# Optimization experiments

Measured on AMD Instinct MI355X. Metric: run time of the kernel, lower is better.

Reference implementation:

```python
import jax, jax.numpy as jnp
import numpy as np

B, T, SD, AD, H, K, HID = 256, 128, 8, 2, 3, 4, 256


def setup_inputs() -> dict:
    key = jax.random.key(0)
    ks = jax.random.split(key, 12)
    inp = {
        "state": jax.random.normal(ks[0], (B, T, SD), dtype=jnp.float32),
        "action": jax.random.normal(ks[1], (B, T, AD), dtype=jnp.float32),
        # Linear(4, 4*H, bias=False): weight (4*H, 4)
        "Wk": jax.random.normal(ks[2], (4 * H, K), dtype=jnp.float32) * 0.1,
        "Wq": jax.random.normal(ks[3], (4 * H, SD + AD), dtype=jnp.float32) * 0.1,
        "Wv": jax.random.normal(ks[4], (4 * H, K), dtype=jnp.float32) * 0.1,
        # MLP: in_dim = 4*H + SD + AD -> HID -> HID -> 1
        "W1": jax.random.normal(ks[5], (HID, 4 * H + SD + AD), dtype=jnp.float32) * 0.05,
        "b1": jnp.zeros((HID,), dtype=jnp.float32),
        "W2": jax.random.normal(ks[6], (HID, HID), dtype=jnp.float32) * 0.05,
        "b2": jnp.zeros((HID,), dtype=jnp.float32),
        "Wout": jax.random.uniform(ks[7], (1, HID), minval=-0.003, maxval=0.003, dtype=jnp.float32),
        "bout": jax.random.uniform(ks[8], (1,), minval=-0.003, maxval=0.003, dtype=jnp.float32),
    }
    return inp


def reference(state, action, Wk, Wq, Wv, W1, b1, W2, b2, Wout, bout):
    q_state = jnp.concatenate([state, action], axis=-1)  # (b, t, sd+ad)
    s = state[:, :, :4]                                   # (b, t, 4)
    b, t, k = s.shape
    h = Wk.shape[0] // k
    # rel_full[b, i, j] = s[b, j] - s[b, i]  (matches torch view/transpose)
    rel_full = s[:, None, :, :] - s[:, :, None, :]        # (b, t, t, 4)
    # drop diagonal (self-pairs): idx[i] = all j != i, in order
    j = jnp.arange(t - 1)
    idx = j[None, :] + (j[None, :] >= jnp.arange(t)[:, None])  # (t, t-1)
    rel = jnp.take_along_axis(rel_full, idx[None, :, :, None], axis=2)  # (b, t, t-1, 4)
    # QKV projections (tiny head dim k=4)
    q = (q_state @ Wq.T).reshape(b, t, h, k)              # (b, t, h, 4)
    keys = (rel @ Wk.T).reshape(b, t, t - 1, h, k)        # (b, t, t-1, h, 4)
    vals = (rel @ Wv.T).reshape(b, t, t - 1, h, k)
    scores = jnp.einsum('bthk,btjhk->bthj', q, keys) / jnp.sqrt(jnp.float32(k))
    w = jax.nn.softmax(scores, axis=-1)                   # over the t-1 neighbors
    x = jnp.einsum('bthj,btjhk->bthk', w, vals).reshape(b, t, h * k)
    x = jnp.concatenate([x, q_state], axis=-1)            # (b, t, h*4 + sd+ad)
    x = jax.nn.relu(x @ W1.T + b1)
    x = jax.nn.relu(x @ W2.T + b2)
    return x @ Wout.T + bout                              # (b, t, 1)
```

## Files before the change

kernel.cpp:

```cpp
#include <hip/hip_runtime.h>
#include <math.h>

#define Bp 256
#define Tp 128
#define SDp 8
#define ADp 2
#define Hp 3
#define Kp 4
#define HIDp 256
#define QDp (SDp + ADp)
#define X1Dp (Hp * Kp + QDp)
#define X1PAD 32
#define H1LD 264
#define LOG2E 1.4426950408889634f

typedef short bf16x8 __attribute__((ext_vector_type(8)));
typedef float f32x4  __attribute__((ext_vector_type(4)));

__device__ __forceinline__ unsigned short f2bf(float f) {
    unsigned u = __float_as_uint(f);
    unsigned r = (u + 0x7FFFu + ((u >> 16) & 1u)) >> 16;
    return (unsigned short)r;
}

__global__ __launch_bounds__(256) void attn_prep_kernel(
    const float* __restrict__ state, const float* __restrict__ action,
    const float* __restrict__ Wk, const float* __restrict__ Wq,
    const float* __restrict__ Wv, const float* __restrict__ W1,
    const float* __restrict__ W2, unsigned short* __restrict__ W1b,
    unsigned short* __restrict__ W2b, unsigned short* __restrict__ X1b)
{
    if (blockIdx.x >= Bp) {
        const int id0 = (blockIdx.x - Bp) * 1024 + threadIdx.x * 4;
        if (id0 < HIDp * HIDp) {
            const float4 v = *(const float4*)(W2 + id0);
            ushort4 o;
            o.x = f2bf(v.x); o.y = f2bf(v.y); o.z = f2bf(v.z); o.w = f2bf(v.w);
            *(ushort4*)(W2b + id0) = o;
        } else {
            #pragma unroll
            for (int u = 0; u < 4; ++u) {
                const int i = id0 - HIDp * HIDp + u;
                const int r = i >> 5, k = i & 31;
                W1b[i] = (k < X1Dp) ? f2bf(W1[r * X1Dp + k]) : (unsigned short)0;
            }
        }
        return;
    }

    const int b  = blockIdx.x;
    const int t  = threadIdx.x & 127;
    const int jh = threadIdx.x >> 7;

    __shared__ float4 s4[Tp];
    __shared__ float  wq[Hp * Kp * QDp];
    __shared__ float  wk[Hp * Kp * Kp];
    __shared__ float  wv[Hp * Kp * Kp];
    __shared__ float  part[Tp][16];

    if (threadIdx.x < Tp)
        s4[threadIdx.x] = ((const float4*)(state + (size_t)b * Tp * SDp))[threadIdx.x * 2];
    if (threadIdx.x >= Tp && threadIdx.x < Tp + Hp * Kp * QDp)
        wq[threadIdx.x - Tp] = Wq[threadIdx.x - Tp];
    if (threadIdx.x < Hp * Kp * Kp) { wk[threadIdx.x] = Wk[threadIdx.x]; wv[threadIdx.x] = Wv[threadIdx.x]; }
    __syncthreads();

    float qs[QDp];
    {
        const float* srow = state + ((size_t)b * Tp + t) * SDp;
        #pragma unroll
        for (int d = 0; d < SDp; ++d) qs[d] = srow[d];
        const float* arow = action + ((size_t)b * Tp + t) * ADp;
        qs[8] = arow[0]; qs[9] = arow[1];
    }

    float q[Hp * Kp];
    #pragma unroll
    for (int r = 0; r < Hp * Kp; ++r) {
        float a = 0.f;
        #pragma unroll
        for (int d = 0; d < QDp; ++d) a += qs[d] * wq[r * QDp + d];
        q[r] = a;
    }
    float qkp[Hp * Kp];
    #pragma unroll
    for (int h = 0; h < Hp; ++h)
        #pragma unroll
        for (int c = 0; c < Kp; ++c) {
            float a = 0.f;
            #pragma unroll
            for (int k = 0; k < Kp; ++k) a += q[h * Kp + k] * wk[(h * Kp + k) * Kp + c];
            qkp[h * Kp + c] = 0.5f * LOG2E * a;
        }

    const float4 st = s4[t];
    float ch[Hp];
    #pragma unroll
    for (int h = 0; h < Hp; ++h)
        ch[h] = st.x * qkp[h*4] + st.y * qkp[h*4+1] + st.z * qkp[h*4+2] + st.w * qkp[h*4+3];

    float l[Hp] = {0.f, 0.f, 0.f};
    float accs[Hp][4] = {};
    const int j0 = jh * 64;
    for (int j = j0; j < j0 + 64; ++j) {
        const float4 sj = s4[j];
        #pragma unroll
        for (int h = 0; h < Hp; ++h) {
            const float d = sj.x * qkp[h*4] + sj.y * qkp[h*4+1]
                          + sj.z * qkp[h*4+2] + sj.w * qkp[h*4+3] - ch[h];
            const float e = (j == t) ? 0.f : exp2f(d);
            l[h] += e;
            accs[h][0] += e * sj.x; accs[h][1] += e * sj.y;
            accs[h][2] += e * sj.z; accs[h][3] += e * sj.w;
        }
    }

    if (jh == 1) {
        #pragma unroll
        for (int h = 0; h < Hp; ++h) {
            part[t][h] = l[h];
            #pragma unroll
            for (int c = 0; c < Kp; ++c) part[t][3 + h * 4 + c] = accs[h][c];
        }
    }
    __syncthreads();

    if (jh == 0) {
        unsigned short rowb[X1PAD];
        #pragma unroll
        for (int h = 0; h < Hp; ++h) {
            const float lt = l[h] + part[t][h];
            const float inv = 1.f / lt;
            const float rb0 = (accs[h][0] + part[t][3 + h*4 + 0]) * inv - st.x;
            const float rb1 = (accs[h][1] + part[t][3 + h*4 + 1]) * inv - st.y;
            const float rb2 = (accs[h][2] + part[t][3 + h*4 + 2]) * inv - st.z;
            const float rb3 = (accs[h][3] + part[t][3 + h*4 + 3]) * inv - st.w;
            #pragma unroll
            for (int k = 0; k < Kp; ++k) {
                const int r = h * Kp + k;
                rowb[r] = f2bf(rb0 * wv[r*4] + rb1 * wv[r*4+1] + rb2 * wv[r*4+2] + rb3 * wv[r*4+3]);
            }
        }
        #pragma unroll
        for (int i = 0; i < QDp; ++i) rowb[Hp * Kp + i] = f2bf(qs[i]);
        #pragma unroll
        for (int i = X1Dp; i < X1PAD; ++i) rowb[i] = 0;

        uint4* dst = (uint4*)(X1b + ((size_t)b * Tp + t) * X1PAD);
        const uint4* srcv = (const uint4*)rowb;
        #pragma unroll
        for (int i = 0; i < 4; ++i) dst[i] = srcv[i];
    }
}

__global__ __launch_bounds__(256, 4) void mlp_kernel(
    const unsigned short* __restrict__ X1b, const unsigned short* __restrict__ W1b,
    const unsigned short* __restrict__ W2b,
    const float* __restrict__ b1, const float* __restrict__ b2,
    const float* __restrict__ Wout, const float* __restrict__ bout,
    float* __restrict__ out)
{
    const int tid  = threadIdx.x;
    const int lane = tid & 63;
    const int wave = tid >> 6;
    const int quad = lane >> 4;
    const int l16  = lane & 15;
    const int pos0 = blockIdx.x * 64;

    __shared__ __align__(16) unsigned short h1s[64 * H1LD];

    {
        const bf16x8 afr = *(const bf16x8*)&X1b[((size_t)pos0 + wave * 16 + l16) * X1PAD + quad * 8];
        for (int nt = 0; nt < 16; ++nt) {
            const bf16x8 bfr = *(const bf16x8*)&W1b[(nt * 16 + l16) * X1PAD + quad * 8];
            f32x4 acc = {0.f, 0.f, 0.f, 0.f};
            acc = __builtin_amdgcn_mfma_f32_16x16x32_bf16(afr, bfr, acc, 0, 0, 0);
            const int col = nt * 16 + l16;
            const float bb = b1[col];
            #pragma unroll
            for (int r = 0; r < 4; ++r)
                h1s[(wave * 16 + quad * 4 + r) * H1LD + col] = f2bf(fmaxf(acc[r] + bb, 0.f));
        }
    }
    __syncthreads();

    bf16x8 A[8];
    #pragma unroll
    for (int ks = 0; ks < 8; ++ks)
        A[ks] = *(const bf16x8*)&h1s[(wave * 16 + l16) * H1LD + ks * 32 + quad * 8];

    float rsum[4] = {0.f, 0.f, 0.f, 0.f};
    for (int nt = 0; nt < 16; ++nt) {
        const int col = nt * 16 + l16;
        const unsigned short* wrow = W2b + (size_t)col * HIDp + quad * 8;
        bf16x8 Bf[8];
        #pragma unroll
        for (int ks = 0; ks < 8; ++ks)
            Bf[ks] = *(const bf16x8*)(wrow + ks * 32);
        f32x4 acc = {0.f, 0.f, 0.f, 0.f};
        #pragma unroll
        for (int ks = 0; ks < 8; ++ks)
            acc = __builtin_amdgcn_mfma_f32_16x16x32_bf16(A[ks], Bf[ks], acc, 0, 0, 0);
        const float bb = b2[col];
        const float wo = Wout[col];
        #pragma unroll
        for (int r = 0; r < 4; ++r)
            rsum[r] += fmaxf(acc[r] + bb, 0.f) * wo;
    }

    #pragma unroll
    for (int off = 1; off < 16; off <<= 1)
        #pragma unroll
        for (int r = 0; r < 4; ++r)
            rsum[r] += __shfl_xor(rsum[r], off, 64);

    if (l16 == 0) {
        const float bo = bout[0];
        #pragma unroll
        for (int r = 0; r < 4; ++r)
            out[pos0 + wave * 16 + quad * 4 + r] = rsum[r] + bo;
    }
}

extern "C" void kernel_launch(void* const* d_in, const int* in_sizes, int n_in,
                              void* d_out, int out_size, void* d_ws, size_t ws_size,
                              hipStream_t stream) {
    const float* state  = (const float*)d_in[0];
    const float* action = (const float*)d_in[1];
    const float* Wk     = (const float*)d_in[2];
    const float* Wq     = (const float*)d_in[3];
    const float* Wv     = (const float*)d_in[4];
    const float* W1     = (const float*)d_in[5];
    const float* b1     = (const float*)d_in[6];
    const float* W2     = (const float*)d_in[7];
    const float* b2     = (const float*)d_in[8];
    const float* Wout   = (const float*)d_in[9];
    const float* bout   = (const float*)d_in[10];
    float* out = (float*)d_out;

    char* ws = (char*)d_ws;
    unsigned short* W1b = (unsigned short*)(ws);
    unsigned short* W2b = (unsigned short*)(ws + 16384);
    unsigned short* X1b = (unsigned short*)(ws + 16384 + 131072);

    attn_prep_kernel<<<Bp + 72, 256, 0, stream>>>(state, action, Wk, Wq, Wv, W1, W2,
                                                  W1b, W2b, X1b);
    mlp_kernel<<<(Bp * Tp) / 64, 256, 0, stream>>>(X1b, W1b, W2b, b1, b2, Wout, bout, out);
}
```

Baseline: 121.0 us.

## Split attention across more blocks and repartition MLP work across waves

The attention kernel now uses four blocks per batch, with 8 threads per query that each cover 16 neighbors and combine their partial sums by shuffle. Per-query projections are computed once into shared memory, and the state is packed to bf16 early. The MLP kernel processes 32 rows per block, and each wave handles a quarter of the W2 columns for both row tiles, so every W2 fragment loaded is reused twice. The intent is more parallelism in the attention stage and fewer redundant W2 global reads. In exchange it adds a cross-wave reduction through shared memory, uses an XOR-swizzled h1 layout to avoid bank conflicts, and uses the fast exp2 intrinsic.

New measurement: 101.3 us. 16.2% less time.

```diff
diff --git a/kernel.cpp b/kernel.cpp
--- a/kernel.cpp
+++ b/kernel.cpp
@@ -10,8 +10,7 @@
 #define HIDp 256
 #define QDp (SDp + ADp)
 #define X1Dp (Hp * Kp + QDp)
-#define X1PAD 32
-#define H1LD 264
+#define QKLD 20
 #define LOG2E 1.4426950408889634f
 
 typedef short bf16x8 __attribute__((ext_vector_type(8)));
@@ -23,118 +22,138 @@
     return (unsigned short)r;
 }
 
-__global__ __launch_bounds__(256) void attn_prep_kernel(
+__device__ __forceinline__ unsigned h1_byte(int row, int colbytes) {
+    return (((unsigned)row << 9) + (unsigned)colbytes) ^ ((unsigned)(row & 7) << 4);
+}
+
+__global__ __launch_bounds__(256, 4) void attn_prep_kernel(
     const float* __restrict__ state, const float* __restrict__ action,
     const float* __restrict__ Wk, const float* __restrict__ Wq,
     const float* __restrict__ Wv, const float* __restrict__ W1,
     const float* __restrict__ W2, unsigned short* __restrict__ W1b,
     unsigned short* __restrict__ W2b, unsigned short* __restrict__ X1b)
 {
-    if (blockIdx.x >= Bp) {
-        const int id0 = (blockIdx.x - Bp) * 1024 + threadIdx.x * 4;
-        if (id0 < HIDp * HIDp) {
-            const float4 v = *(const float4*)(W2 + id0);
+    const int tid = threadIdx.x;
+    if (blockIdx.x >= 1024) {
+        const int pb = blockIdx.x - 1024;
+        if (pb < 64) {
+            const int i = pb * 1024 + tid * 4;
+            const float4 v = *(const float4*)(W2 + i);
             ushort4 o;
             o.x = f2bf(v.x); o.y = f2bf(v.y); o.z = f2bf(v.z); o.w = f2bf(v.w);
-            *(ushort4*)(W2b + id0) = o;
+            *(ushort4*)(W2b + i) = o;
         } else {
-            #pragma unroll
-            for (int u = 0; u < 4; ++u) {
-                const int i = id0 - HIDp * HIDp + u;
-                const int r = i >> 5, k = i & 31;
-                W1b[i] = (k < X1Dp) ? f2bf(W1[r * X1Dp + k]) : (unsigned short)0;
-            }
+            const int i = (pb - 64) * 256 + tid;
+            const int r = i >> 5, c = i & 31;
+            W1b[i] = (c < X1Dp) ? f2bf(W1[r * X1Dp + c]) : (unsigned short)0;
         }
         return;
     }
 
-    const int b  = blockIdx.x;
-    const int t  = threadIdx.x & 127;
-    const int jh = threadIdx.x >> 7;
+    const int bid   = blockIdx.x;
+    const int batch = bid >> 2;
+    const int t0    = (bid & 3) * 32;
+    const int t_loc = tid >> 3;
+    const int jo    = tid & 7;
+    const int t     = t0 + t_loc;
 
     __shared__ float4 s4[Tp];
     __shared__ float  wq[Hp * Kp * QDp];
     __shared__ float  wk[Hp * Kp * Kp];
     __shared__ float  wv[Hp * Kp * Kp];
-    __shared__ float  part[Tp][16];
-
-    if (threadIdx.x < Tp)
-        s4[threadIdx.x] = ((const float4*)(state + (size_t)b * Tp * SDp))[threadIdx.x * 2];
-    if (threadIdx.x >= Tp && threadIdx.x < Tp + Hp * Kp * QDp)
-        wq[threadIdx.x - Tp] = Wq[threadIdx.x - Tp];
-    if (threadIdx.x < Hp * Kp * Kp) { wk[threadIdx.x] = Wk[threadIdx.x]; wv[threadIdx.x] = Wv[threadIdx.x]; }
-    __syncthreads();
-
-    float qs[QDp];
-    {
-        const float* srow = state + ((size_t)b * Tp + t) * SDp;
-        #pragma unroll
-        for (int d = 0; d < SDp; ++d) qs[d] = srow[d];
-        const float* arow = action + ((size_t)b * Tp + t) * ADp;
-        qs[8] = arow[0]; qs[9] = arow[1];
-    }
-
-    float q[Hp * Kp];
-    #pragma unroll
-    for (int r = 0; r < Hp * Kp; ++r) {
-        float a = 0.f;
-        #pragma unroll
-        for (int d = 0; d < QDp; ++d) a += qs[d] * wq[r * QDp + d];
-        q[r] = a;
-    }
-    float qkp[Hp * Kp];
-    #pragma unroll
-    for (int h = 0; h < Hp; ++h)
-        #pragma unroll
-        for (int c = 0; c < Kp; ++c) {
+    __shared__ float  qk[32 * QKLD];
+
+    if (tid < Tp)
+        s4[tid] = ((const float4*)(state + (size_t)batch * Tp * SDp))[tid * 2];
+    if (tid >= Tp && tid < Tp + Hp * Kp * QDp)
+        wq[tid - Tp] = Wq[tid - Tp];
+    if (tid < Hp * Kp * Kp) { wk[tid] = Wk[tid]; wv[tid] = Wv[tid]; }
+    __syncthreads();
+
+    if (tid < 32) {
+        const int tt = t0 + tid;
+        const float* srow = state + ((size_t)batch * Tp + tt) * SDp;
+        float qs[QDp];
+        {
+            const float4 v0 = *(const float4*)srow;
+            const float4 v1 = *(const float4*)(srow + 4);
+            qs[0]=v0.x; qs[1]=v0.y; qs[2]=v0.z; qs[3]=v0.w;
+            qs[4]=v1.x; qs[5]=v1.y; qs[6]=v1.z; qs[7]=v1.w;
+            const float* arow = action + ((size_t)batch * Tp + tt) * ADp;
+            qs[8] = arow[0]; qs[9] = arow[1];
+        }
+        float q[Hp * Kp];
+        #pragma unroll
+        for (int r = 0; r < Hp * Kp; ++r) {
             float a = 0.f;
             #pragma unroll
-            for (int k = 0; k < Kp; ++k) a += q[h * Kp + k] * wk[(h * Kp + k) * Kp + c];
-            qkp[h * Kp + c] = 0.5f * LOG2E * a;
-        }
-
-    const float4 st = s4[t];
-    float ch[Hp];
-    #pragma unroll
-    for (int h = 0; h < Hp; ++h)
-        ch[h] = st.x * qkp[h*4] + st.y * qkp[h*4+1] + st.z * qkp[h*4+2] + st.w * qkp[h*4+3];
+            for (int d = 0; d < QDp; ++d) a += qs[d] * wq[r * QDp + d];
+            q[r] = a;
+        }
+        float* qrow = &qk[tid * QKLD];
+        const float4 st = s4[tt];
+        #pragma unroll
+        for (int h = 0; h < Hp; ++h) {
+            float p[4];
+            #pragma unroll
+            for (int c = 0; c < Kp; ++c) {
+                float a = 0.f;
+                #pragma unroll
+                for (int k = 0; k < Kp; ++k) a += q[h * Kp + k] * wk[(h * Kp + k) * Kp + c];
+                p[c] = 0.5f * LOG2E * a;
+                qrow[h * 4 + c] = p[c];
+            }
+            qrow[12 + h] = st.x * p[0] + st.y * p[1] + st.z * p[2] + st.w * p[3];
+        }
+        #pragma unroll
+        for (int i = 0; i < 5; ++i) {
+            const unsigned u = (unsigned)f2bf(qs[2*i]) | ((unsigned)f2bf(qs[2*i+1]) << 16);
+            qrow[15 + i] = __uint_as_float(u);
+        }
+    }
+    __syncthreads();
+
+    float rq[20];
+    #pragma unroll
+    for (int i = 0; i < 5; ++i)
+        *(float4*)&rq[i * 4] = *(const float4*)&qk[t_loc * QKLD + i * 4];
 
     float l[Hp] = {0.f, 0.f, 0.f};
-    float accs[Hp][4] = {};
-    const int j0 = jh * 64;
-    for (int j = j0; j < j0 + 64; ++j) {
+    float ac[Hp][4] = {};
+    #pragma unroll
+    for (int i = 0; i < 16; ++i) {
+        const int j = (jo << 4) | ((i + jo) & 15);
         const float4 sj = s4[j];
         #pragma unroll
         for (int h = 0; h < Hp; ++h) {
-            const float d = sj.x * qkp[h*4] + sj.y * qkp[h*4+1]
-                          + sj.z * qkp[h*4+2] + sj.w * qkp[h*4+3] - ch[h];
-            const float e = (j == t) ? 0.f : exp2f(d);
+            const float d = sj.x * rq[h*4] + sj.y * rq[h*4+1]
+                          + sj.z * rq[h*4+2] + sj.w * rq[h*4+3] - rq[12 + h];
+            const float e = (j == t) ? 0.f : __builtin_amdgcn_exp2f(d);
             l[h] += e;
-            accs[h][0] += e * sj.x; accs[h][1] += e * sj.y;
-            accs[h][2] += e * sj.z; accs[h][3] += e * sj.w;
-        }
-    }
-
-    if (jh == 1) {
-        #pragma unroll
-        for (int h = 0; h < Hp; ++h) {
-            part[t][h] = l[h];
-            #pragma unroll
-            for (int c = 0; c < Kp; ++c) part[t][3 + h * 4 + c] = accs[h][c];
-        }
-    }
-    __syncthreads();
-
-    if (jh == 0) {
-        unsigned short rowb[X1PAD];
-        #pragma unroll
-        for (int h = 0; h < Hp; ++h) {
-            const float lt = l[h] + part[t][h];
-            const float inv = 1.f / lt;
-            const float rb0 = (accs[h][0] + part[t][3 + h*4 + 0]) * inv - st.x;
-            const float rb1 = (accs[h][1] + part[t][3 + h*4 + 1]) * inv - st.y;
-            const float rb2 = (accs[h][2] + part[t][3 + h*4 + 2]) * inv - st.z;
-            const float rb3 = (accs[h][3] + part[t][3 + h*4 + 3]) * inv - st.w;
+            ac[h][0] += e * sj.x; ac[h][1] += e * sj.y;
+            ac[h][2] += e * sj.z; ac[h][3] += e * sj.w;
+        }
+    }
+    #pragma unroll
+    for (int off = 1; off < 8; off <<= 1) {
+        #pragma unroll
+        for (int h = 0; h < Hp; ++h) {
+            l[h] += __shfl_xor(l[h], off);
+            #pragma unroll
+            for (int c = 0; c < Kp; ++c) ac[h][c] += __shfl_xor(ac[h][c], off);
+        }
+    }
+
+    if (jo == 0) {
+        const float4 st = s4[t];
+        unsigned short rowb[32] __attribute__((aligned(16)));
+        #pragma unroll
+        for (int h = 0; h < Hp; ++h) {
+            const float inv = 1.f / l[h];
+            const float rb0 = ac[h][0] * inv - st.x;
+            const float rb1 = ac[h][1] * inv - st.y;
+            const float rb2 = ac[h][2] * inv - st.z;
+            const float rb3 = ac[h][3] * inv - st.w;
             #pragma unroll
             for (int k = 0; k < Kp; ++k) {
                 const int r = h * Kp + k;
@@ -142,18 +161,22 @@
             }
         }
         #pragma unroll
-        for (int i = 0; i < QDp; ++i) rowb[Hp * Kp + i] = f2bf(qs[i]);
-        #pragma unroll
-        for (int i = X1Dp; i < X1PAD; ++i) rowb[i] = 0;
-
-        uint4* dst = (uint4*)(X1b + ((size_t)b * Tp + t) * X1PAD);
+        for (int i = 0; i < 5; ++i) {
+            const unsigned u = __float_as_uint(rq[15 + i]);
+            rowb[12 + 2*i] = (unsigned short)(u & 0xffffu);
+            rowb[13 + 2*i] = (unsigned short)(u >> 16);
+        }
+        #pragma unroll
+        for (int i = X1Dp; i < 32; ++i) rowb[i] = 0;
+
+        uint4* dst = (uint4*)(X1b + ((size_t)batch * Tp + t) * 32);
         const uint4* srcv = (const uint4*)rowb;
         #pragma unroll
         for (int i = 0; i < 4; ++i) dst[i] = srcv[i];
     }
 }
 
-__global__ __launch_bounds__(256, 4) void mlp_kernel(
+__global__ __launch_bounds__(256, 3) void mlp_kernel(
     const unsigned short* __restrict__ X1b, const unsigned short* __restrict__ W1b,
     const unsigned short* __restrict__ W2b,
     const float* __restrict__ b1, const float* __restrict__ b2,
@@ -165,60 +188,83 @@
     const int wave = tid >> 6;
     const int quad = lane >> 4;
     const int l16  = lane & 15;
-    const int pos0 = blockIdx.x * 64;
-
-    __shared__ __align__(16) unsigned short h1s[64 * H1LD];
+    const int pos0 = blockIdx.x * 32;
+
+    __shared__ __align__(16) unsigned short h1s[32 * 256];
+    __shared__ float partial[4][32];
 
     {
-        const bf16x8 afr = *(const bf16x8*)&X1b[((size_t)pos0 + wave * 16 + l16) * X1PAD + quad * 8];
-        for (int nt = 0; nt < 16; ++nt) {
-            const bf16x8 bfr = *(const bf16x8*)&W1b[(nt * 16 + l16) * X1PAD + quad * 8];
+        const int rt  = wave & 1;
+        const int chh = wave >> 1;
+        const bf16x8 afr = *(const bf16x8*)&X1b[((size_t)pos0 + rt * 16 + l16) * 32 + quad * 8];
+        #pragma unroll
+        for (int n8 = 0; n8 < 8; ++n8) {
+            const int col = chh * 128 + n8 * 16 + l16;
+            const bf16x8 bfr = *(const bf16x8*)&W1b[col * 32 + quad * 8];
             f32x4 acc = {0.f, 0.f, 0.f, 0.f};
             acc = __builtin_amdgcn_mfma_f32_16x16x32_bf16(afr, bfr, acc, 0, 0, 0);
-            const int col = nt * 16 + l16;
             const float bb = b1[col];
             #pragma unroll
-            for (int r = 0; r < 4; ++r)
-                h1s[(wave * 16 + quad * 4 + r) * H1LD + col] = f2bf(fmaxf(acc[r] + bb, 0.f));
-        }
-    }
-    __syncthreads();
-
-    bf16x8 A[8];
-    #pragma unroll
-    for (int ks = 0; ks < 8; ++ks)
-        A[ks] = *(const bf16x8*)&h1s[(wave * 16 + l16) * H1LD + ks * 32 + quad * 8];
-
-    float rsum[4] = {0.f, 0.f, 0.f, 0.f};
-    for (int nt = 0; nt < 16; ++nt) {
-        const int col = nt * 16 + l16;
-        const unsigned short* wrow = W2b + (size_t)col * HIDp + quad * 8;
+            for (int r = 0; r < 4; ++r) {
+                const int row = rt * 16 + quad * 4 + r;
+                *(unsigned short*)((char*)h1s + h1_byte(row, col * 2)) =
+                    f2bf(fmaxf(acc[r] + bb, 0.f));
+            }
+        }
+    }
+    __syncthreads();
+
+    bf16x8 A[2][8];
+    #pragma unroll
+    for (int rt2 = 0; rt2 < 2; ++rt2)
+        #pragma unroll
+        for (int ks = 0; ks < 8; ++ks)
+            A[rt2][ks] = *(const bf16x8*)((const char*)h1s +
+                           h1_byte(rt2 * 16 + l16, ks * 64 + quad * 16));
+
+    float rsum[2][4] = {};
+    #pragma unroll
+    for (int i = 0; i < 4; ++i) {
+        const int col = (wave * 4 + i) * 16 + l16;
+        const unsigned short* wr = W2b + (size_t)col * HIDp + quad * 8;
         bf16x8 Bf[8];
         #pragma unroll
         for (int ks = 0; ks < 8; ++ks)
-            Bf[ks] = *(const bf16x8*)(wrow + ks * 32);
-        f32x4 acc = {0.f, 0.f, 0.f, 0.f};
-        #pragma unroll
-        for (int ks = 0; ks < 8; ++ks)
-            acc = __builtin_amdgcn_mfma_f32_16x16x32_bf16(A[ks], Bf[ks], acc, 0, 0, 0);
+            Bf[ks] = *(const bf16x8*)(wr + ks * 32);
         const float bb = b2[col];
         const float wo = Wout[col];
         #pragma unroll
-        for (int r = 0; r < 4; ++r)
-            rsum[r] += fmaxf(acc[r] + bb, 0.f) * wo;
+        for (int rt2 = 0; rt2 < 2; ++rt2) {
+            f32x4 acc = {0.f, 0.f, 0.f, 0.f};
+            #pragma unroll
+            for (int ks = 0; ks < 8; ++ks)
+                acc = __builtin_amdgcn_mfma_f32_16x16x32_bf16(A[rt2][ks], Bf[ks], acc, 0, 0, 0);
+            #pragma unroll
+            for (int r = 0; r < 4; ++r)
+                rsum[rt2][r] += fmaxf(acc[r] + bb, 0.f) * wo;
+        }
     }
 
     #pragma unroll
     for (int off = 1; off < 16; off <<= 1)
         #pragma unroll
-        for (int r = 0; r < 4; ++r)
-            rsum[r] += __shfl_xor(rsum[r], off, 64);
+        for (int rt2 = 0; rt2 < 2; ++rt2)
+            #pragma unroll
+            for (int r = 0; r < 4; ++r)
+                rsum[rt2][r] += __shfl_xor(rsum[rt2][r], off);
 
     if (l16 == 0) {
-        const float bo = bout[0];
-        #pragma unroll
-        for (int r = 0; r < 4; ++r)
-            out[pos0 + wave * 16 + quad * 4 + r] = rsum[r] + bo;
+        #pragma unroll
+        for (int rt2 = 0; rt2 < 2; ++rt2)
+            #pragma unroll
+            for (int r = 0; r < 4; ++r)
+                partial[wave][rt2 * 16 + quad * 4 + r] = rsum[rt2][r];
+    }
+    __syncthreads();
+
+    if (tid < 32) {
+        out[pos0 + tid] = partial[0][tid] + partial[1][tid]
+                        + partial[2][tid] + partial[3][tid] + bout[0];
     }
 }
 
@@ -243,7 +289,8 @@
     unsigned short* W2b = (unsigned short*)(ws + 16384);
     unsigned short* X1b = (unsigned short*)(ws + 16384 + 131072);
 
-    attn_prep_kernel<<<Bp + 72, 256, 0, stream>>>(state, action, Wk, Wq, Wv, W1, W2,
-                                                  W1b, W2b, X1b);
-    mlp_kernel<<<(Bp * Tp) / 64, 256, 0, stream>>>(X1b, W1b, W2b, b1, b2, Wout, bout, out);
-}
+    attn_prep_kernel<<<1024 + 96, 256, 0, stream>>>(state, action, Wk, Wq, Wv,
+                                                    W1, W2, W1b, W2b, X1b);
+    mlp_kernel<<<(Bp * Tp) / 32, 256, 0, stream>>>(X1b, W1b, W2b, b1, b2,
+                                                   Wout, bout, out);
+}
```
